# Kernel tuning notes

Measured on AMD Instinct MI355X. Metric: run time of the kernel, lower is better.

The kernel has to match this reference:

```python
import jax, jax.numpy as jnp
import numpy as np

EMBED = 1024
HEADS = 16
HEAD_DIM = EMBED // HEADS
RANK = 8
ALPHA = 16
SCALE_LORA = ALPHA / RANK  # 2.0


def _lora_linear(x, W, b, A, B):
    # F.linear(x, W, b) + scale * F.linear(F.linear(x, A), B)
    return x @ W.T + b + SCALE_LORA * ((x @ A.T) @ B.T)


def setup_inputs() -> dict:
    key = jax.random.key(0)
    ks = jax.random.split(key, 17)
    d = {"x": jax.random.normal(ks[0], (2, 2048, EMBED), dtype=jnp.float32)}
    names = ["q", "k", "v", "o"]
    i = 1
    for n in names:
        d[f"W{n}"] = jax.random.normal(ks[i], (EMBED, EMBED), dtype=jnp.float32) * 0.02; i += 1
        d[f"b{n}"] = jnp.zeros((EMBED,), dtype=jnp.float32)
        d[f"A{n}"] = jax.random.normal(ks[i], (RANK, EMBED), dtype=jnp.float32) * 0.02; i += 1
        d[f"B{n}"] = jax.random.normal(ks[i], (EMBED, RANK), dtype=jnp.float32) * 0.02; i += 1
    return d


def reference(x, Wq, bq, Aq, Bq, Wk, bk, Ak, Bk, Wv, bv, Av, Bv, Wo, bo, Ao, Bo):
    N, S, _ = x.shape
    Q = _lora_linear(x, Wq, bq, Aq, Bq).reshape(N, S, HEADS, HEAD_DIM)
    K = _lora_linear(x, Wk, bk, Ak, Bk).reshape(N, S, HEADS, HEAD_DIM)
    V = _lora_linear(x, Wv, bv, Av, Bv).reshape(N, S, HEADS, HEAD_DIM)
    # energy: [N, H, Sq, Sk]
    energy = jnp.einsum("nqhd,nkhd->nhqk", Q, K) / jnp.sqrt(jnp.float32(HEAD_DIM))
    attn = jax.nn.softmax(energy, axis=-1)
    out = jnp.einsum("nhqk,nkhd->nqhd", attn, V).reshape(N, S, EMBED)
    return _lora_linear(out, Wo, bo, Ao, Bo)
```

## Files before the change

kernel.cpp:

```cpp
#include <hip/hip_runtime.h>
#include <stdint.h>

typedef uint16_t u16;
typedef short s16x8 __attribute__((ext_vector_type(8)));
typedef float f32x4 __attribute__((ext_vector_type(4)));
typedef unsigned short u16x4 __attribute__((ext_vector_type(4)));
typedef uint32_t u32;
typedef u32 u32x2 __attribute__((ext_vector_type(2)));

#define MFMA16(a,b,c) __builtin_amdgcn_mfma_f32_16x16x32_bf16((a),(b),(c),0,0,0)
#define QSCALE 0.18033688011112042f

__device__ __forceinline__ float b2f(u16 b){
  union { u32 u; float f; } v; v.u = ((u32)b)<<16; return v.f;
}
__device__ __forceinline__ u16 f2b(float f){
  union { float f; u32 u; } v; v.f = f;
  return (u16)((v.u + 0x7fffu + ((v.u>>16)&1u))>>16);
}
__device__ __forceinline__ u32 fbits(float f){
  union { float f; u32 u; } v; v.f = f; return v.u;
}
__device__ __forceinline__ float trunc_bf(float f){
  union { u32 u; float f; } v; v.u = fbits(f) & 0xffff0000u; return v.f;
}
__device__ __forceinline__ void load_lds_16B(const void* g, void* l){
  __builtin_amdgcn_global_load_lds((const __attribute__((address_space(1))) void*)g,
                                   (__attribute__((address_space(3))) void*)l, 16, 0, 0);
}

__global__ __launch_bounds__(256) void convert_kernel(
    const float* __restrict__ W0, const float* __restrict__ W1,
    const float* __restrict__ W2, const float* __restrict__ W3,
    u16* __restrict__ Wb)
{
  const int y = blockIdx.y;
  const float* src = (y==0)?W0:(y==1)?W1:(y==2)?W2:W3;
  u16* dst = Wb + (size_t)y*1048576;
  const int g = blockIdx.x*256 + threadIdx.x;
#pragma unroll
  for (int t=0;t<4;t++){
    const int i4 = g + t*65536;
    const f32x4 v = *(const f32x4*)(src + (size_t)i4*4);
    u16x4 o;
#pragma unroll
    for (int j=0;j<4;j++) o[j] = f2b(v[j]);
    *(u16x4*)(dst + (size_t)i4*4) = o;
  }
}

template<bool XF32, int NMAT>
__global__ __launch_bounds__(256) void lora_t_kernel(
    const void* __restrict__ Xv,
    const float* __restrict__ A0, const float* __restrict__ A1, const float* __restrict__ A2,
    float* __restrict__ T0, float* __restrict__ T1, float* __restrict__ T2,
    u16* __restrict__ xb)
{
  const int wid = threadIdx.x>>6, lane = threadIdx.x&63;
  const int m = blockIdx.x*4 + wid;

  float xf[16];
  if (XF32){
    const float* xp = (const float*)Xv + (size_t)m*1024 + lane*16;
#pragma unroll
    for (int q=0;q<4;q++){
      const f32x4 v = *(const f32x4*)(xp + q*4);
#pragma unroll
      for (int j=0;j<4;j++) xf[q*4+j] = v[j];
    }
    u16* xbp = xb + (size_t)m*1024 + lane*16;
#pragma unroll
    for (int q=0;q<4;q++){
      u16x4 o;
#pragma unroll
      for (int j=0;j<4;j++) o[j] = f2b(xf[q*4+j]);
      *(u16x4*)(xbp + q*4) = o;
    }
  } else {
    const u16* xp = (const u16*)Xv + (size_t)m*1024 + lane*16;
#pragma unroll
    for (int j=0;j<16;j++) xf[j] = b2f(xp[j]);
  }

#pragma unroll
  for (int mat=0; mat<NMAT; mat++){
    const float* A = (mat==0)?A0:(mat==1)?A1:A2;
    float* T = (mat==0)?T0:(mat==1)?T1:T2;
    float accv[8];
#pragma unroll
    for (int r=0;r<8;r++){
      const float* ap = A + r*1024 + lane*16;
      float s = 0.f;
#pragma unroll
      for (int q=0;q<4;q++){
        const f32x4 av = *(const f32x4*)(ap + q*4);
#pragma unroll
        for (int j=0;j<4;j++) s += xf[q*4+j]*av[j];
      }
      accv[r] = s;
    }
#pragma unroll
    for (int r=0;r<8;r++){
      float s = accv[r];
      s += __shfl_xor(s,1);  s += __shfl_xor(s,2);  s += __shfl_xor(s,4);
      s += __shfl_xor(s,8);  s += __shfl_xor(s,16); s += __shfl_xor(s,32);
      accv[r] = s;
    }
    if (lane==0){
#pragma unroll
      for (int r=0;r<8;r++) T[(size_t)m*8 + r] = accv[r];
    }
  }
}

__global__ __launch_bounds__(256,2) void gemm_qkv_kernel(
    const u16* __restrict__ Xb, const u16* __restrict__ Wb,
    const float* __restrict__ bq, const float* __restrict__ bk, const float* __restrict__ bv,
    const float* __restrict__ tq, const float* __restrict__ tk, const float* __restrict__ tv,
    const float* __restrict__ Blq, const float* __restrict__ Blk, const float* __restrict__ Blv,
    u16* __restrict__ Qb, u16* __restrict__ Kb, u16* __restrict__ Vtb)
{
  __shared__ u16 At[128*32];
  __shared__ u16 Bt[128*32];
  const int tid = threadIdx.x;
  const int wid = tid>>6, lane = tid&63;
  const int quad = lane>>4, l16 = lane&15;
  const int wm = wid>>1, wn = wid&1;
  const int proj = blockIdx.x>>3;
  const int n0 = (blockIdx.x&7)<<7, m0 = blockIdx.y<<7;
  const u16* W = Wb + (size_t)proj*1048576;
  const float* bias = (proj==0)?bq:(proj==1)?bk:bv;
  const float* T    = (proj==0)?tq:(proj==1)?tk:tv;
  const float* Bl   = (proj==0)?Blq:(proj==1)?Blk:Blv;
  const float scale = (proj==0)?QSCALE:1.0f;

  f32x4 acc[4][4];
#pragma unroll
  for (int i=0;i<4;i++)
#pragma unroll
    for (int j=0;j<4;j++) acc[i][j] = f32x4{0.f,0.f,0.f,0.f};

  for (int k0=0;k0<1024;k0+=32){
#pragma unroll
    for (int p=0;p<2;p++){
      const int s = wid*128 + p*64 + lane;
      const int row = s>>2, c = s&3;
      load_lds_16B(Xb + (size_t)(m0+row)*1024 + k0 + c*8, At + (wid*128+p*64)*8);
      load_lds_16B(W  + (size_t)(n0+row)*1024 + k0 + c*8, Bt + (wid*128+p*64)*8);
    }
    __syncthreads();
    s16x8 af[4], bfr[4];
#pragma unroll
    for (int t=0;t<4;t++){
      const int r = wm*64 + t*16 + l16;
      af[t]  = *(const s16x8*)(At + r*32 + quad*8);
      const int c = wn*64 + t*16 + l16;
      bfr[t] = *(const s16x8*)(Bt + c*32 + quad*8);
    }
#pragma unroll
    for (int tm=0;tm<4;tm++)
#pragma unroll
      for (int tn=0;tn<4;tn++)
        acc[tm][tn] = MFMA16(af[tm], bfr[tn], acc[tm][tn]);
    __syncthreads();
  }

  s16x8 tf[4], bfl[4];
#pragma unroll
  for (int t=0;t<4;t++){ tf[t] = s16x8{0,0,0,0,0,0,0,0}; bfl[t] = s16x8{0,0,0,0,0,0,0,0}; }
  if (quad==0){
#pragma unroll
    for (int tm=0;tm<4;tm++){
      const float* tp = T + (size_t)(m0 + wm*64 + tm*16 + l16)*8;
      const f32x4 a0 = *(const f32x4*)(tp);
      const f32x4 a1 = *(const f32x4*)(tp+4);
#pragma unroll
      for (int j=0;j<4;j++){ tf[tm][j] = (short)f2b(2.0f*a0[j]); tf[tm][4+j] = (short)f2b(2.0f*a1[j]); }
    }
#pragma unroll
    for (int tn=0;tn<4;tn++){
      const float* bp = Bl + (size_t)(n0 + wn*64 + tn*16 + l16)*8;
      const f32x4 b0 = *(const f32x4*)(bp);
      const f32x4 b1 = *(const f32x4*)(bp+4);
#pragma unroll
      for (int j=0;j<4;j++){ bfl[tn][j] = (short)f2b(b0[j]); bfl[tn][4+j] = (short)f2b(b1[j]); }
    }
  }
#pragma unroll
  for (int tm=0;tm<4;tm++)
#pragma unroll
    for (int tn=0;tn<4;tn++)
      acc[tm][tn] = MFMA16(tf[tm], bfl[tn], acc[tm][tn]);

#pragma unroll
  for (int tn=0;tn<4;tn++){
    const int n = n0 + wn*64 + tn*16 + l16;
    const float bn = bias[n];
#pragma unroll
    for (int tm=0;tm<4;tm++){
      const int mb = m0 + wm*64 + tm*16 + quad*4;
      if (proj==0){
#pragma unroll
        for (int rg=0;rg<4;rg++) Qb[(size_t)(mb+rg)*1024 + n] = f2b((acc[tm][tn][rg]+bn)*scale);
      } else if (proj==1){
#pragma unroll
        for (int rg=0;rg<4;rg++) Kb[(size_t)(mb+rg)*1024 + n] = f2b(acc[tm][tn][rg]+bn);
      } else {
        const int batch = mb>>11, sI = mb&2047;
        const int hh = n>>6, dd = n&63;
        u16x4 pk;
#pragma unroll
        for (int rg=0;rg<4;rg++) pk[rg] = f2b(acc[tm][tn][rg]+bn);
        *(u16x4*)(Vtb + (size_t)((batch*16+hh)*64+dd)*2048 + sI) = pk;
      }
    }
  }
}

__global__ __launch_bounds__(256,2) void gemm_o_kernel(
    const u16* __restrict__ Xb, const u16* __restrict__ W,
    const float* __restrict__ bias, const float* __restrict__ T,
    const float* __restrict__ Bl, float* __restrict__ Out)
{
  __shared__ u16 At[128*32];
  __shared__ u16 Bt[64*32];
  const int tid = threadIdx.x;
  const int wid = tid>>6, lane = tid&63;
  const int quad = lane>>4, l16 = lane&15;
  const int wm = wid>>1, wn = wid&1;
  const int m0 = blockIdx.y<<7, n0 = blockIdx.x<<6;

  f32x4 acc[4][2];
#pragma unroll
  for (int i=0;i<4;i++)
#pragma unroll
    for (int j=0;j<2;j++) acc[i][j] = f32x4{0.f,0.f,0.f,0.f};

  for (int k0=0;k0<1024;k0+=32){
#pragma unroll
    for (int p=0;p<2;p++){
      const int s = wid*128 + p*64 + lane;
      const int row = s>>2, c = s&3;
      load_lds_16B(Xb + (size_t)(m0+row)*1024 + k0 + c*8, At + (wid*128+p*64)*8);
    }
    { const int s = wid*64 + lane;
      const int row = s>>2, c = s&3;
      load_lds_16B(W + (size_t)(n0+row)*1024 + k0 + c*8, Bt + (wid*64)*8); }
    __syncthreads();
    s16x8 af[4], bfr[2];
#pragma unroll
    for (int t=0;t<4;t++){
      const int r = wm*64 + t*16 + l16;
      af[t] = *(const s16x8*)(At + r*32 + quad*8);
    }
#pragma unroll
    for (int t=0;t<2;t++){
      const int c = wn*32 + t*16 + l16;
      bfr[t] = *(const s16x8*)(Bt + c*32 + quad*8);
    }
#pragma unroll
    for (int tm=0;tm<4;tm++)
#pragma unroll
      for (int tn=0;tn<2;tn++)
        acc[tm][tn] = MFMA16(af[tm], bfr[tn], acc[tm][tn]);
    __syncthreads();
  }

  s16x8 tf[4], bfl[2];
#pragma unroll
  for (int t=0;t<4;t++) tf[t] = s16x8{0,0,0,0,0,0,0,0};
#pragma unroll
  for (int t=0;t<2;t++) bfl[t] = s16x8{0,0,0,0,0,0,0,0};
  if (quad==0){
#pragma unroll
    for (int tm=0;tm<4;tm++){
      const float* tp = T + (size_t)(m0 + wm*64 + tm*16 + l16)*8;
      const f32x4 a0 = *(const f32x4*)(tp);
      const f32x4 a1 = *(const f32x4*)(tp+4);
#pragma unroll
      for (int j=0;j<4;j++){ tf[tm][j] = (short)f2b(2.0f*a0[j]); tf[tm][4+j] = (short)f2b(2.0f*a1[j]); }
    }
#pragma unroll
    for (int tn=0;tn<2;tn++){
      const float* bp = Bl + (size_t)(n0 + wn*32 + tn*16 + l16)*8;
      const f32x4 b0 = *(const f32x4*)(bp);
      const f32x4 b1 = *(const f32x4*)(bp+4);
#pragma unroll
      for (int j=0;j<4;j++){ bfl[tn][j] = (short)f2b(b0[j]); bfl[tn][4+j] = (short)f2b(b1[j]); }
    }
  }
#pragma unroll
  for (int tm=0;tm<4;tm++)
#pragma unroll
    for (int tn=0;tn<2;tn++)
      acc[tm][tn] = MFMA16(tf[tm], bfl[tn], acc[tm][tn]);

#pragma unroll
  for (int tn=0;tn<2;tn++){
    const int n = n0 + wn*32 + tn*16 + l16;
    const float bn = bias[n];
#pragma unroll
    for (int tm=0;tm<4;tm++){
      const int mb = m0 + wm*64 + tm*16 + quad*4;
#pragma unroll
      for (int rg=0;rg<4;rg++)
        Out[(size_t)(mb+rg)*1024 + n] = acc[tm][tn][rg] + bn;
    }
  }
}

__global__ __launch_bounds__(256,2) void attn_kernel(
    const u16* __restrict__ Q, const u16* __restrict__ K,
    const u16* __restrict__ Vt, u16* __restrict__ Out)
{
  __shared__ u16 Kt[128*72];
  __shared__ u16 Vtl[64*136];
  __shared__ u16 Pt[128*136];
  const int tid = threadIdx.x;
  const int wid = tid>>6, lane = tid&63;
  const int quad = lane>>4, l16 = lane&15;
  const int q0 = blockIdx.x<<7;
  const int h = blockIdx.y, nb = blockIdx.z;
  const int qw = wid*32;

  s16x8 qf[2][2];
#pragma unroll
  for (int g=0;g<2;g++){
    const int row = q0 + qw + g*16 + l16;
#pragma unroll
    for (int dh=0;dh<2;dh++)
      qf[g][dh] = *(const s16x8*)(Q + (size_t)(nb*2048+row)*1024 + h*64 + dh*32 + quad*8);
  }
  f32x4 OT[2][4];
  float lr[2] = {0.f, 0.f};
#pragma unroll
  for (int g=0;g<2;g++)
#pragma unroll
    for (int td=0;td<4;td++) OT[g][td] = f32x4{0.f,0.f,0.f,0.f};

  s16x8 kreg[4], vreg[4];
#pragma unroll
  for (int p=0;p<4;p++){
    const int s = p*256 + tid;
    { const int row = s>>3, c = s&7;
      kreg[p] = *(const s16x8*)(K + (size_t)(nb*2048+row)*1024 + h*64 + c*8); }
    { const int row = s>>4, c = s&15;
      vreg[p] = *(const s16x8*)(Vt + (size_t)((nb*16+h)*64+row)*2048 + c*8); }
  }

  for (int kt=0; kt<2048; kt+=128){
#pragma unroll
    for (int p=0;p<4;p++){
      const int s = p*256 + tid;
      { const int row = s>>3, c = s&7;
        *(s16x8*)(Kt + row*72 + c*8) = kreg[p]; }
      { const int row = s>>4, c = s&15;
        *(s16x8*)(Vtl + row*136 + c*8) = vreg[p]; }
    }
    __syncthreads();

    if (kt < 2048-128){
      const int kn = kt + 128;
#pragma unroll
      for (int p=0;p<4;p++){
        const int s = p*256 + tid;
        { const int row = s>>3, c = s&7;
          kreg[p] = *(const s16x8*)(K + (size_t)(nb*2048+kn+row)*1024 + h*64 + c*8); }
        { const int row = s>>4, c = s&15;
          vreg[p] = *(const s16x8*)(Vt + (size_t)((nb*16+h)*64+row)*2048 + kn + c*8); }
      }
    }

#pragma unroll
    for (int tn=0;tn<8;tn++){
      const int key = tn*16 + l16;
      const s16x8 kf0 = *(const s16x8*)(Kt + key*72 + quad*8);
      const s16x8 kf1 = *(const s16x8*)(Kt + key*72 + 32 + quad*8);
#pragma unroll
      for (int g=0;g<2;g++){
        f32x4 z = f32x4{0.f,0.f,0.f,0.f};
        z = MFMA16(kf0, qf[g][0], z);
        z = MFMA16(kf1, qf[g][1], z);
        float p0 = __builtin_amdgcn_exp2f(z[0]);
        float p1 = __builtin_amdgcn_exp2f(z[1]);
        float p2 = __builtin_amdgcn_exp2f(z[2]);
        float p3 = __builtin_amdgcn_exp2f(z[3]);
        lr[g] += (trunc_bf(p0)+trunc_bf(p1)) + (trunc_bf(p2)+trunc_bf(p3));
        u32x2 pk;
        pk[0] = __builtin_amdgcn_perm(fbits(p1), fbits(p0), 0x07060302u);
        pk[1] = __builtin_amdgcn_perm(fbits(p3), fbits(p2), 0x07060302u);
        *(u32x2*)(Pt + (qw+g*16+l16)*136 + tn*16 + quad*4) = pk;
      }
    }

    __builtin_amdgcn_s_setprio(1);
#pragma unroll
    for (int kb=0;kb<4;kb++){
      s16x8 pf[2];
#pragma unroll
      for (int g=0;g<2;g++)
        pf[g] = *(const s16x8*)(Pt + (qw+g*16+l16)*136 + kb*32 + quad*8);
#pragma unroll
      for (int td=0;td<4;td++){
        const s16x8 vf = *(const s16x8*)(Vtl + (td*16+l16)*136 + kb*32 + quad*8);
#pragma unroll
        for (int g=0;g<2;g++)
          OT[g][td] = MFMA16(vf, pf[g], OT[g][td]);
      }
    }
    __builtin_amdgcn_s_setprio(0);
    __syncthreads();
  }

#pragma unroll
  for (int g=0;g<2;g++){
    float t = lr[g];
    t += __shfl_xor(t,16);
    t += __shfl_xor(t,32);
    const float linv = 1.0f / t;
    const int q = q0 + qw + g*16 + l16;
#pragma unroll
    for (int td=0;td<4;td++){
      u16x4 pk;
#pragma unroll
      for (int rg=0;rg<4;rg++) pk[rg] = f2b(OT[g][td][rg]*linv);
      *(u16x4*)(Out + (size_t)(nb*2048+q)*1024 + h*64 + td*16 + quad*4) = pk;
    }
  }
}

extern "C" void kernel_launch(void* const* d_in, const int* in_sizes, int n_in,
                              void* d_out, int out_size, void* d_ws, size_t ws_size,
                              hipStream_t stream)
{
  const float* x  = (const float*)d_in[0];
  const float* Wq = (const float*)d_in[1];  const float* bq = (const float*)d_in[2];
  const float* Aq = (const float*)d_in[3];  const float* Bq = (const float*)d_in[4];
  const float* Wk = (const float*)d_in[5];  const float* bk = (const float*)d_in[6];
  const float* Ak = (const float*)d_in[7];  const float* Bk = (const float*)d_in[8];
  const float* Wv = (const float*)d_in[9];  const float* bv = (const float*)d_in[10];
  const float* Av = (const float*)d_in[11]; const float* Bv = (const float*)d_in[12];
  const float* Wo = (const float*)d_in[13]; const float* bo = (const float*)d_in[14];
  const float* Ao = (const float*)d_in[15]; const float* Bo = (const float*)d_in[16];

  char* ws = (char*)d_ws;
  float* tq = (float*)(ws + 0);
  float* tk = (float*)(ws + 131072);
  float* tv = (float*)(ws + 262144);
  float* to = (float*)(ws + 393216);
  u16* xb  = (u16*)(ws + 524288);
  u16* Ab  = xb;
  u16* Wb  = (u16*)(ws + 524288 + 8388608);
  u16* Qb  = (u16*)(ws + 524288 + 2*8388608);
  u16* Kb  = (u16*)(ws + 524288 + 3*8388608);
  u16* Vtb = (u16*)(ws + 524288 + 4*8388608);

  lora_t_kernel<true,3><<<dim3(1024),256,0,stream>>>(x, Aq, Ak, Av, tq, tk, tv, xb);
  convert_kernel<<<dim3(256,4),256,0,stream>>>(Wq, Wk, Wv, Wo, Wb);
  gemm_qkv_kernel<<<dim3(24,32),256,0,stream>>>(xb, Wb, bq, bk, bv, tq, tk, tv,
                                                Bq, Bk, Bv, Qb, Kb, Vtb);
  attn_kernel<<<dim3(16,16,2),256,0,stream>>>(Qb, Kb, Vtb, Ab);
  lora_t_kernel<false,1><<<dim3(1024),256,0,stream>>>(Ab, Ao, Ao, Ao, to, to, to, nullptr);
  gemm_o_kernel<<<dim3(16,32),256,0,stream>>>(Ab, Wb + (size_t)3*1048576, bo, to, Bo,
                                              (float*)d_out);
}
```

Before: 244.9 us.

## Keep attention probabilities in registers via permlane swaps, double-buffer K/V tiles, fuse weight conversion

Attention now converts the score MFMA outputs into the P operand layout in registers using permlane32/permlane16 swaps, instead of writing P to shared memory and reading it back. K/V tiles are double-buffered in LDS, which removes one barrier per iteration and lets global loads run two tiles ahead. The weight fp32-to-bf16 conversion is merged into the LoRA-T kernel as extra blocks, saving one launch. The trade-offs are higher register pressure from the prefetch and a lane-permutation mapping that must match the MFMA operand layout exactly.

```diff
diff --git a/kernel.cpp b/kernel.cpp
--- a/kernel.cpp
+++ b/kernel.cpp
@@ -7,6 +7,7 @@
 typedef unsigned short u16x4 __attribute__((ext_vector_type(4)));
 typedef uint32_t u32;
 typedef u32 u32x2 __attribute__((ext_vector_type(2)));
+typedef u32 u32x4 __attribute__((ext_vector_type(4)));
 
 #define MFMA16(a,b,c) __builtin_amdgcn_mfma_f32_16x16x32_bf16((a),(b),(c),0,0,0)
 #define QSCALE 0.18033688011112042f
@@ -29,33 +30,34 @@
                                    (__attribute__((address_space(3))) void*)l, 16, 0, 0);
 }
 
-__global__ __launch_bounds__(256) void convert_kernel(
+template<bool XF32, int NMAT>
+__global__ __launch_bounds__(256) void lora_conv_kernel(
+    const void* __restrict__ Xv,
+    const float* __restrict__ A0, const float* __restrict__ A1, const float* __restrict__ A2,
+    float* __restrict__ T0, float* __restrict__ T1, float* __restrict__ T2,
+    u16* __restrict__ xb,
     const float* __restrict__ W0, const float* __restrict__ W1,
     const float* __restrict__ W2, const float* __restrict__ W3,
     u16* __restrict__ Wb)
 {
-  const int y = blockIdx.y;
-  const float* src = (y==0)?W0:(y==1)?W1:(y==2)?W2:W3;
-  u16* dst = Wb + (size_t)y*1048576;
-  const int g = blockIdx.x*256 + threadIdx.x;
-#pragma unroll
-  for (int t=0;t<4;t++){
-    const int i4 = g + t*65536;
-    const f32x4 v = *(const f32x4*)(src + (size_t)i4*4);
-    u16x4 o;
-#pragma unroll
-    for (int j=0;j<4;j++) o[j] = f2b(v[j]);
-    *(u16x4*)(dst + (size_t)i4*4) = o;
-  }
-}
-
-template<bool XF32, int NMAT>
-__global__ __launch_bounds__(256) void lora_t_kernel(
-    const void* __restrict__ Xv,
-    const float* __restrict__ A0, const float* __restrict__ A1, const float* __restrict__ A2,
-    float* __restrict__ T0, float* __restrict__ T1, float* __restrict__ T2,
-    u16* __restrict__ xb)
-{
+  if (XF32 && blockIdx.x >= 1024){
+    const int cv = blockIdx.x - 1024;
+    const int y = cv>>8;
+    const float* src = (y==0)?W0:(y==1)?W1:(y==2)?W2:W3;
+    u16* dst = Wb + (size_t)y*1048576;
+    const int g = (cv&255)*256 + threadIdx.x;
+#pragma unroll
+    for (int t=0;t<4;t++){
+      const int i4 = g + t*65536;
+      const f32x4 v = *(const f32x4*)(src + (size_t)i4*4);
+      u16x4 o;
+#pragma unroll
+      for (int j=0;j<4;j++) o[j] = f2b(v[j]);
+      *(u16x4*)(dst + (size_t)i4*4) = o;
+    }
+    return;
+  }
+
   const int wid = threadIdx.x>>6, lane = threadIdx.x&63;
   const int m = blockIdx.x*4 + wid;
 
@@ -313,9 +315,8 @@
     const u16* __restrict__ Q, const u16* __restrict__ K,
     const u16* __restrict__ Vt, u16* __restrict__ Out)
 {
-  __shared__ u16 Kt[128*72];
-  __shared__ u16 Vtl[64*136];
-  __shared__ u16 Pt[128*136];
+  __shared__ u16 KtB[2][128*72];
+  __shared__ u16 VtB[2][64*136];
   const int tid = threadIdx.x;
   const int wid = tid>>6, lane = tid&63;
   const int quad = lane>>4, l16 = lane&15;
@@ -339,76 +340,79 @@
     for (int td=0;td<4;td++) OT[g][td] = f32x4{0.f,0.f,0.f,0.f};
 
   s16x8 kreg[4], vreg[4];
-#pragma unroll
-  for (int p=0;p<4;p++){
-    const int s = p*256 + tid;
-    { const int row = s>>3, c = s&7;
-      kreg[p] = *(const s16x8*)(K + (size_t)(nb*2048+row)*1024 + h*64 + c*8); }
-    { const int row = s>>4, c = s&15;
-      vreg[p] = *(const s16x8*)(Vt + (size_t)((nb*16+h)*64+row)*2048 + c*8); }
-  }
-
-  for (int kt=0; kt<2048; kt+=128){
+  auto LOADT = [&](int kn){
 #pragma unroll
     for (int p=0;p<4;p++){
       const int s = p*256 + tid;
-      { const int row = s>>3, c = s&7;
-        *(s16x8*)(Kt + row*72 + c*8) = kreg[p]; }
-      { const int row = s>>4, c = s&15;
-        *(s16x8*)(Vtl + row*136 + c*8) = vreg[p]; }
-    }
-    __syncthreads();
-
-    if (kt < 2048-128){
-      const int kn = kt + 128;
-#pragma unroll
-      for (int p=0;p<4;p++){
-        const int s = p*256 + tid;
-        { const int row = s>>3, c = s&7;
-          kreg[p] = *(const s16x8*)(K + (size_t)(nb*2048+kn+row)*1024 + h*64 + c*8); }
-        { const int row = s>>4, c = s&15;
-          vreg[p] = *(const s16x8*)(Vt + (size_t)((nb*16+h)*64+row)*2048 + kn + c*8); }
+      kreg[p] = *(const s16x8*)(K + (size_t)(nb*2048+kn+(s>>3))*1024 + h*64 + (s&7)*8);
+      vreg[p] = *(const s16x8*)(Vt + (size_t)((nb*16+h)*64+(s>>4))*2048 + kn + (s&15)*8);
+    }
+  };
+  auto WRITET = [&](int b){
+    u16* Ktb = KtB[b]; u16* Vtb = VtB[b];
+#pragma unroll
+    for (int p=0;p<4;p++){
+      const int s = p*256 + tid;
+      *(s16x8*)(Ktb + (s>>3)*72 + (s&7)*8) = kreg[p];
+      *(s16x8*)(Vtb + (s>>4)*136 + (s&15)*8) = vreg[p];
+    }
+  };
+
+  LOADT(0);
+  WRITET(0);
+  LOADT(128);
+  __syncthreads();
+
+  for (int t=0;t<16;t++){
+    const int cur = t&1;
+    if (t < 15) WRITET(cur^1);
+    if (t < 14) LOADT((t+2)*128);
+    const u16* KtC = KtB[cur];
+    const u16* VtC = VtB[cur];
+
+#pragma unroll
+    for (int kb=0;kb<4;kb++){
+      u32 ew[2][2], ow[2][2];
+#pragma unroll
+      for (int sel=0;sel<2;sel++){
+        const int key = (kb*2+sel)*16 + l16;
+        const s16x8 kf0 = *(const s16x8*)(KtC + key*72 + quad*8);
+        const s16x8 kf1 = *(const s16x8*)(KtC + key*72 + 32 + quad*8);
+#pragma unroll
+        for (int g=0;g<2;g++){
+          f32x4 z = f32x4{0.f,0.f,0.f,0.f};
+          z = MFMA16(kf0, qf[g][0], z);
+          z = MFMA16(kf1, qf[g][1], z);
+          const float p0 = __builtin_amdgcn_exp2f(z[0]);
+          const float p1 = __builtin_amdgcn_exp2f(z[1]);
+          const float p2 = __builtin_amdgcn_exp2f(z[2]);
+          const float p3 = __builtin_amdgcn_exp2f(z[3]);
+          lr[g] += (trunc_bf(p0)+trunc_bf(p1)) + (trunc_bf(p2)+trunc_bf(p3));
+          const u32 w0 = __builtin_amdgcn_perm(fbits(p1), fbits(p0), 0x07060302u);
+          const u32 w1 = __builtin_amdgcn_perm(fbits(p3), fbits(p2), 0x07060302u);
+          if (sel==0){ ew[g][0]=w0; ew[g][1]=w1; } else { ow[g][0]=w0; ow[g][1]=w1; }
+        }
       }
-    }
-
-#pragma unroll
-    for (int tn=0;tn<8;tn++){
-      const int key = tn*16 + l16;
-      const s16x8 kf0 = *(const s16x8*)(Kt + key*72 + quad*8);
-      const s16x8 kf1 = *(const s16x8*)(Kt + key*72 + 32 + quad*8);
+      s16x8 pf[2];
 #pragma unroll
       for (int g=0;g<2;g++){
-        f32x4 z = f32x4{0.f,0.f,0.f,0.f};
-        z = MFMA16(kf0, qf[g][0], z);
-        z = MFMA16(kf1, qf[g][1], z);
-        float p0 = __builtin_amdgcn_exp2f(z[0]);
-        float p1 = __builtin_amdgcn_exp2f(z[1]);
-        float p2 = __builtin_amdgcn_exp2f(z[2]);
-        float p3 = __builtin_amdgcn_exp2f(z[3]);
-        lr[g] += (trunc_bf(p0)+trunc_bf(p1)) + (trunc_bf(p2)+trunc_bf(p3));
-        u32x2 pk;
-        pk[0] = __builtin_amdgcn_perm(fbits(p1), fbits(p0), 0x07060302u);
-        pk[1] = __builtin_amdgcn_perm(fbits(p3), fbits(p2), 0x07060302u);
-        *(u32x2*)(Pt + (qw+g*16+l16)*136 + tn*16 + quad*4) = pk;
+        const u32x2 r32 = __builtin_amdgcn_permlane32_swap(ew[g][0], ow[g][0], false, false);
+        const u32x2 r16 = __builtin_amdgcn_permlane16_swap(r32[0], r32[1], false, false);
+        const u32x2 s32 = __builtin_amdgcn_permlane32_swap(ew[g][1], ow[g][1], false, false);
+        const u32x2 s16v = __builtin_amdgcn_permlane16_swap(s32[0], s32[1], false, false);
+        u32x4 pw; pw[0]=r16[0]; pw[1]=s16v[0]; pw[2]=r16[1]; pw[3]=s16v[1];
+        pf[g] = __builtin_bit_cast(s16x8, pw);
       }
-    }
-
-    __builtin_amdgcn_s_setprio(1);
-#pragma unroll
-    for (int kb=0;kb<4;kb++){
-      s16x8 pf[2];
-#pragma unroll
-      for (int g=0;g<2;g++)
-        pf[g] = *(const s16x8*)(Pt + (qw+g*16+l16)*136 + kb*32 + quad*8);
+      __builtin_amdgcn_s_setprio(1);
 #pragma unroll
       for (int td=0;td<4;td++){
-        const s16x8 vf = *(const s16x8*)(Vtl + (td*16+l16)*136 + kb*32 + quad*8);
+        const s16x8 vf = *(const s16x8*)(VtC + (td*16+l16)*136 + kb*32 + quad*8);
 #pragma unroll
         for (int g=0;g<2;g++)
           OT[g][td] = MFMA16(vf, pf[g], OT[g][td]);
       }
-    }
-    __builtin_amdgcn_s_setprio(0);
+      __builtin_amdgcn_s_setprio(0);
+    }
     __syncthreads();
   }
 
@@ -455,12 +459,14 @@
   u16* Kb  = (u16*)(ws + 524288 + 3*8388608);
   u16* Vtb = (u16*)(ws + 524288 + 4*8388608);
 
-  lora_t_kernel<true,3><<<dim3(1024),256,0,stream>>>(x, Aq, Ak, Av, tq, tk, tv, xb);
-  convert_kernel<<<dim3(256,4),256,0,stream>>>(Wq, Wk, Wv, Wo, Wb);
+  lora_conv_kernel<true,3><<<dim3(2048),256,0,stream>>>(
+      x, Aq, Ak, Av, tq, tk, tv, xb, Wq, Wk, Wv, Wo, Wb);
   gemm_qkv_kernel<<<dim3(24,32),256,0,stream>>>(xb, Wb, bq, bk, bv, tq, tk, tv,
                                                 Bq, Bk, Bv, Qb, Kb, Vtb);
   attn_kernel<<<dim3(16,16,2),256,0,stream>>>(Qb, Kb, Vtb, Ab);
-  lora_t_kernel<false,1><<<dim3(1024),256,0,stream>>>(Ab, Ao, Ao, Ao, to, to, to, nullptr);
+  lora_conv_kernel<false,1><<<dim3(1024),256,0,stream>>>(
+      Ab, Ao, Ao, Ao, to, to, to, nullptr,
+      nullptr, nullptr, nullptr, nullptr, nullptr);
   gemm_o_kernel<<<dim3(16,32),256,0,stream>>>(Ab, Wb + (size_t)3*1048576, bo, to, Bo,
                                               (float*)d_out);
 }
```

Result: no change. 242.7 us (-0.9%).
